# Kernel tuning notes

Measured on AMD Instinct MI355X. Metric: run time of the kernel, lower is better.

## Reference

```python
import jax, jax.numpy as jnp
import numpy as np

N_EL, N_NUC, N_UP = 768, 32, 384
EMB, EDGE_IN, TPS = 128, 32, 64
N_SAME = 2 * N_UP * (N_UP - 1)   # 294144
N_ANTI = 2 * N_UP * N_UP         # 294912
N_NE = N_NUC * N_EL              # 24576


def silu(x):
    return x * jax.nn.sigmoid(x)


def setup_inputs() -> dict:
    key = jax.random.key(0)
    ks = iter(jax.random.split(key, 32))
    r = lambda shape: jax.random.normal(next(ks), shape, jnp.float32)
    ri = lambda shape, hi: jax.random.randint(next(ks), shape, 0, hi, jnp.int32)
    return dict(
        electrons=r((N_EL, EMB)),
        nuclei=r((N_NUC, TPS)),
        feat_same=r((N_SAME, EDGE_IN)),
        feat_anti=r((N_ANTI, EDGE_IN)),
        feat_ne=r((N_NE, EDGE_IN)),
        senders_same=ri((N_SAME,), N_EL),
        receivers_same=ri((N_SAME,), N_EL),
        senders_anti=ri((N_ANTI,), N_EL),
        receivers_anti=ri((N_ANTI,), N_EL),
        senders_ne=ri((N_NE,), N_NUC),
        receivers_ne=ri((N_NE,), N_EL),
        # stacked subnet params, edge-type order: (same, anti, ne)
        u_W=r((3, EDGE_IN, TPS)) * 0.1, u_b=r((3, TPS)) * 0.1,
        w_W=r((3, TPS, TPS)) * 0.1, w_b=r((3, TPS)) * 0.1,
        h_W_ee=r((2, EMB, TPS)) * 0.1, h_b_ee=r((2, TPS)) * 0.1,  # same, anti
        h_W_ne=r((TPS, TPS)) * 0.1, h_b_ne=r((TPS,)) * 0.1,
        g_W_res=r((EMB, EMB)) * 0.1, g_b_res=r((EMB,)) * 0.1,
        g_W_z=r((3, TPS, EMB)) * 0.1, g_b_z=r((3, EMB)) * 0.1,
    )


def reference(electrons, nuclei, feat_same, feat_anti, feat_ne,
              senders_same, receivers_same, senders_anti, receivers_anti,
              senders_ne, receivers_ne,
              u_W, u_b, w_W, w_b, h_W_ee, h_b_ee, h_W_ne, h_b_ne,
              g_W_res, g_b_res, g_W_z, g_b_z):
    n_el = electrons.shape[0]
    feats = (feat_same, feat_anti, feat_ne)
    senders = (senders_same, senders_anti, senders_ne)
    receivers = (receivers_same, receivers_anti, receivers_ne)
    # h subnet applied to sender node data (electrons for same/anti, nuclei for ne)
    hx_nodes = (
        silu(electrons @ h_W_ee[0] + h_b_ee[0]),
        silu(electrons @ h_W_ee[1] + h_b_ee[1]),
        silu(nuclei @ h_W_ne + h_b_ne),
    )
    z = []
    for t in range(3):  # fixed structural loop over edge types
        e = silu(feats[t] @ u_W[t] + u_b[t])     # deep edge features: u[typ]
        we = silu(e @ w_W[t] + w_b[t])           # w[typ](edge.features)
        msg = we * hx_nodes[t][senders[t]]       # convolution: gather + elementwise
        z.append(jax.ops.segment_sum(msg, receivers[t], num_segments=n_el))
    # featurewise update rule: g_residual(electrons) + sum_typ g_typ(z[typ])
    updated = silu(electrons @ g_W_res + g_b_res)
    for t in range(3):
        updated = updated + silu(z[t] @ g_W_z[t] + g_b_z[t])
    # residual connection on electron embeddings
    return updated + electrons
```

## Files before the change

### kernel.cpp

```cpp
#include <hip/hip_runtime.h>
#include <hip/hip_bf16.h>
#include <stdint.h>

#define N_ELx 768
#define EMBx 128
#define TPSx 64
#define EDGE_INx 32
#define EPB 512
#define NBINS 2304
#define NB_SORT 96

typedef __attribute__((ext_vector_type(8))) short bf16x8;
typedef __attribute__((ext_vector_type(4))) float f32x4;
typedef __attribute__((ext_vector_type(4))) uint32_t u32x4;

__device__ __forceinline__ short f2bf(float f) {
    union { float f; uint32_t u; } v; v.f = f;
    uint32_t u = v.u;
    uint32_t r = (u + 0x7FFFu + ((u >> 16) & 1u)) >> 16;
    return (short)r;
}

__device__ __forceinline__ uint32_t cvtpk(float lo, float hi) {
    uint32_t r;
    asm("v_cvt_pk_bf16_f32 %0, %1, %2" : "=v"(r) : "v"(lo), "v"(hi));
    return r;
}

__device__ __forceinline__ bf16x8 mk8(uint32_t a, uint32_t b, uint32_t c, uint32_t d) {
    union { u32x4 u; bf16x8 h; } x;
    x.u = (u32x4){a, b, c, d};
    return x.h;
}

__device__ __forceinline__ float silu_f(float x) {
    float e = __builtin_amdgcn_exp2f(-1.442695041f * x);
    return x * __builtin_amdgcn_rcpf(1.0f + e);
}

__global__ __launch_bounds__(256)
void setup_kernel(const float* __restrict__ elec, const float* __restrict__ nuclei,
                  const float* __restrict__ uW, const float* __restrict__ wW,
                  const float* __restrict__ hWee, const float* __restrict__ hbee,
                  const float* __restrict__ hWne, const float* __restrict__ hbne,
                  float* __restrict__ hx0, float* __restrict__ hx1, float* __restrict__ hxn,
                  short* __restrict__ ufragT, short* __restrict__ wWfrag,
                  const int* __restrict__ r0, const int* __restrict__ r1,
                  const int* __restrict__ r2,
                  int n0, int n1, int n2, int* __restrict__ blockHist,
                  float* __restrict__ z)
{
    __shared__ __align__(16) char smem[32768];
    int b = blockIdx.x;
    int tid = threadIdx.x;
    if (b < 12) {
        short* lds_a = (short*)smem;
        int t = b / 6, rb = b % 6;
        const float* W = hWee + t * (128 * 64);
        {
            int row = tid >> 1, half = tid & 1;
            const float4* src = (const float4*)(elec + (size_t)(rb * 128 + row) * 128 + half * 64);
            #pragma unroll
            for (int c = 0; c < 8; ++c) {
                float4 fa = src[c * 2 + 0], fb = src[c * 2 + 1];
                bf16x8 v;
                v[0] = f2bf(fa.x); v[1] = f2bf(fa.y); v[2] = f2bf(fa.z); v[3] = f2bf(fa.w);
                v[4] = f2bf(fb.x); v[5] = f2bf(fb.y); v[6] = f2bf(fb.z); v[7] = f2bf(fb.w);
                int kk = half * 2 + (c >> 2), kc = c & 3;
                *(bf16x8*)&lds_a[((kk * 4 + kc) * 128 + row) * 8] = v;
            }
        }
        __syncthreads();
        int lane = tid & 63, w = tid >> 6, kc = lane >> 4, cr = lane & 15;
        int col = w * 16 + cr;
        bf16x8 bfrag[4];
        #pragma unroll
        for (int kk = 0; kk < 4; ++kk) {
            bf16x8 v;
            #pragma unroll
            for (int j = 0; j < 8; ++j)
                v[j] = f2bf(W[(kk * 32 + kc * 8 + j) * 64 + col]);
            bfrag[kk] = v;
        }
        float bias = hbee[t * 64 + col];
        float* dst = (t == 0 ? hx0 : hx1);
        f32x4 zero4 = {0.f, 0.f, 0.f, 0.f};
        #pragma unroll
        for (int rt = 0; rt < 8; ++rt) {
            f32x4 acc = zero4;
            #pragma unroll
            for (int kk = 0; kk < 4; ++kk) {
                bf16x8 a = *(const bf16x8*)&lds_a[((kk * 4 + kc) * 128 + rt * 16 + cr) * 8];
                acc = __builtin_amdgcn_mfma_f32_16x16x32_bf16(a, bfrag[kk], acc, 0, 0, 0);
            }
            #pragma unroll
            for (int r = 0; r < 4; ++r) {
                int row = rb * 128 + rt * 16 + kc * 4 + r;
                dst[row * 64 + col] = silu_f(acc[r] + bias);
            }
        }
    } else if (b == 12) {
        int lr = tid >> 6, col = tid & 63;
        for (int i = 0; i < 8; ++i) {
            int row = lr * 8 + i;
            float acc = 0.f;
            for (int k = 0; k < 64; ++k)
                acc += nuclei[row * 64 + k] * hWne[k * 64 + col];
            hxn[row * 64 + col] = silu_f(acc + hbne[col]);
        }
    } else if (b == 13) {
        for (int idx = tid; idx < 3 * 4 * 64; idx += 256) {
            int lane = idx & 63, tr = (idx >> 6) & 3, ty = idx >> 8;
            int lg = lane >> 4, cr = lane & 15;
            for (int j = 0; j < 8; ++j)
                ufragT[idx * 8 + j] =
                    f2bf(uW[(ty * EDGE_INx + lg * 8 + j) * TPSx + tr * 16 + cr]);
        }
        for (int idx = tid; idx < 3 * 2 * 4 * 64; idx += 256) {
            int lane = idx & 63, ct = (idx >> 6) & 3, ks = (idx >> 8) & 1, ty = idx >> 9;
            for (int j = 0; j < 8; ++j) {
                int k = ks * 32 + (lane >> 4) * 8 + j, col = ct * 16 + (lane & 15);
                wWfrag[idx * 8 + j] = f2bf(wW[(ty * 64 + k) * 64 + col]);
            }
        }
    } else {
        int* h = (int*)smem;
        int bb = b - 14;
        for (int i = bb * 256 + tid; i < 3 * N_ELx * TPSx; i += NB_SORT * 256)
            z[i] = 0.f;
        for (int i = tid; i < NBINS; i += 256) h[i] = 0;
        __syncthreads();
        int total = n0 + n1 + n2;
        int chunk = (total + NB_SORT - 1) / NB_SORT;
        int start = bb * chunk, end = min(start + chunk, total);
        for (int i = start + tid; i < end; i += 256) {
            int t, j;
            if (i < n0)            { t = 0; j = i; }
            else if (i < n0 + n1)  { t = 1; j = i - n0; }
            else                   { t = 2; j = i - n0 - n1; }
            int rv = (t == 0 ? r0 : (t == 1 ? r1 : r2))[j];
            atomicAdd(&h[t * 768 + rv], 1);
        }
        __syncthreads();
        for (int i = tid; i < NBINS; i += 256)
            blockHist[i * NB_SORT + bb] = h[i];
    }
}

__global__ __launch_bounds__(256)
void binscan_kernel(int* __restrict__ blockHist, int* __restrict__ binTotal)
{
    int bin = blockIdx.x * 256 + threadIdx.x;
    int* p = blockHist + bin * NB_SORT;
    int run = 0;
    for (int b = 0; b < NB_SORT; ++b) { int v = p[b]; p[b] = run; run += v; }
    binTotal[bin] = run;
}

__global__ __launch_bounds__(256)
void scatter2_kernel(const int* __restrict__ r0, const int* __restrict__ r1,
                     const int* __restrict__ r2,
                     int n0, int n1, int n2,
                     const int* __restrict__ blockHist,
                     const int* __restrict__ binTotal,
                     int* __restrict__ perm)
{
    __shared__ int cursor[NBINS];
    __shared__ int part[256];
    int tid = threadIdx.x, b = blockIdx.x;
    int l[9]; int s = 0;
    #pragma unroll
    for (int j = 0; j < 9; ++j) { l[j] = binTotal[tid * 9 + j]; s += l[j]; }
    part[tid] = s;
    __syncthreads();
    for (int off = 1; off < 256; off <<= 1) {
        int v = (tid >= off) ? part[tid - off] : 0;
        __syncthreads();
        part[tid] += v;
        __syncthreads();
    }
    int run = (tid == 0) ? 0 : part[tid - 1];
    #pragma unroll
    for (int j = 0; j < 9; ++j) {
        int bin = tid * 9 + j;
        cursor[bin] = run + blockHist[bin * NB_SORT + b];
        run += l[j];
    }
    __syncthreads();
    int total = n0 + n1 + n2;
    int chunk = (total + NB_SORT - 1) / NB_SORT;
    int start = b * chunk, end = min(start + chunk, total);
    for (int i = start + tid; i < end; i += 256) {
        int t, j;
        if (i < n0)            { t = 0; j = i; }
        else if (i < n0 + n1)  { t = 1; j = i - n0; }
        else                   { t = 2; j = i - n0 - n1; }
        int rv = (t == 0 ? r0 : (t == 1 ? r1 : r2))[j];
        int pos = atomicAdd(&cursor[t * 768 + rv], 1);
        perm[pos] = j;
    }
}

__global__ __launch_bounds__(256)
void edge_kernel(const float* __restrict__ feat0, const float* __restrict__ feat1,
                 const float* __restrict__ feat2,
                 const int* __restrict__ s0, const int* __restrict__ s1, const int* __restrict__ s2,
                 const int* __restrict__ r0, const int* __restrict__ r1, const int* __restrict__ r2,
                 const float* __restrict__ u_b, const float* __restrict__ w_b,
                 const float* __restrict__ hx0, const float* __restrict__ hx1,
                 const float* __restrict__ hxn,
                 const short* __restrict__ ufragT, const short* __restrict__ wWfrag,
                 const int* __restrict__ perm,
                 float* __restrict__ z,
                 int n0, int n1, int n2, int nb0, int nb1)
{
    int b = blockIdx.x;
    int t; const float* feat; const int* sn; const int* rc; const float* hx; int nE;
    if (b < nb0)            { t = 0; feat = feat0; sn = s0; rc = r0; hx = hx0; nE = n0; }
    else if (b < nb0 + nb1) { t = 1; b -= nb0; feat = feat1; sn = s1; rc = r1; hx = hx1; nE = n1; }
    else                    { t = 2; b -= nb0 + nb1; feat = feat2; sn = s2; rc = r2; hx = hxn; nE = n2; }

    int tid = threadIdx.x;
    int w = tid >> 6, lane = tid & 63, lg = lane >> 4, cr = lane & 15;
    int ebase = b * EPB + w * 128;
    if (ebase >= nE) return;
    bool partial = (ebase + 128 > nE);
    int t_off = (t == 0) ? 0 : (t == 1 ? n0 : n0 + n1);
    float* zt = z + t * (N_ELx * TPSx);

    bf16x8 uf[4];
    #pragma unroll
    for (int tr = 0; tr < 4; ++tr)
        uf[tr] = *(const bf16x8*)(ufragT + ((t * 4 + tr) * 64 + lane) * 8);
    bf16x8 wf[4][2];
    #pragma unroll
    for (int tn = 0; tn < 4; ++tn)
        #pragma unroll
        for (int ks = 0; ks < 2; ++ks)
            wf[tn][ks] = *(const bf16x8*)(wWfrag + (((t * 2 + ks) * 4 + tn) * 64 + lane) * 8);
    float4 ubv[4];
    #pragma unroll
    for (int tr = 0; tr < 4; ++tr)
        ubv[tr] = *(const float4*)(u_b + t * 64 + tr * 16 + lg * 4);
    float wbv[4];
    #pragma unroll
    for (int tn = 0; tn < 4; ++tn)
        wbv[tn] = w_b[t * 64 + tn * 16 + cr];

    int pe_own0, pe_own1, s_own0, s_own1, r_own0, r_own1;
    {
        int e0i = ebase + lane;
        int e1i = ebase + 64 + lane;
        pe_own0 = perm[t_off + min(e0i, nE - 1)];
        pe_own1 = perm[t_off + min(e1i, nE - 1)];
        s_own0 = sn[pe_own0]; r_own0 = rc[pe_own0];
        s_own1 = sn[pe_own1]; r_own1 = rc[pe_own1];
    }

    const int srcA = ((lg & 1) * 2) * 16 + cr;
    const int srcB = srcA + 16;
    const bool selLow = (lg < 2);
    f32x4 zero4 = {0.f, 0.f, 0.f, 0.f};

    float accv[4] = {0.f, 0.f, 0.f, 0.f};
    int curR = -1;
    auto flush = [&]() {
        if (curR >= 0) {
            #pragma unroll
            for (int tn = 0; tn < 4; ++tn) {
                float v = accv[tn];
                v += __shfl_xor(v, 16, 64);
                v += __shfl_xor(v, 32, 64);
                if (lg == 0) atomicAdd(&zt[curR * 64 + tn * 16 + cr], v);
                accv[tn] = 0.f;
            }
        }
    };

    int pF_n = __shfl(pe_own0, cr, 64);
    float4 fa_n, fc_n;
    {
        const float4* fp = (const float4*)(feat + (size_t)pF_n * EDGE_INx + lg * 8);
        fa_n = fp[0]; fc_n = fp[1];
    }

    #pragma unroll 2
    for (int tc = 0; tc < 8; ++tc) {
        int slot_hi = (tc & 4);
        int b16 = (tc & 3) * 16;
        float4 fa = fa_n, fc = fc_n;

        if (tc < 7) {
            int ntc = tc + 1;
            int npe = ((ntc & 4)) ? pe_own1 : pe_own0;
            pF_n = __shfl(npe, ((ntc & 3) * 16) + cr, 64);
            const float4* fp = (const float4*)(feat + (size_t)pF_n * EDGE_INx + lg * 8);
            fa_n = fp[0]; fc_n = fp[1];
        }

        int s_cur = slot_hi ? s_own1 : s_own0;
        int r_cur = slot_hi ? r_own1 : r_own0;
        int sidv[4];
        #pragma unroll
        for (int r = 0; r < 4; ++r)
            sidv[r] = __shfl(s_cur, b16 + lg * 4 + r, 64);
        int rF = __shfl(r_cur, b16, 64);
        int rL = __shfl(r_cur, b16 + 15, 64);

        float hv[4][4];
        if (!partial) {
            #pragma unroll
            for (int r = 0; r < 4; ++r) {
                const float* hp = hx + sidv[r] * TPSx + cr;
                #pragma unroll
                for (int tn = 0; tn < 4; ++tn)
                    hv[tn][r] = hp[tn * 16];
            }
        } else {
            #pragma unroll
            for (int r = 0; r < 4; ++r) {
                bool aE = (ebase + tc * 16 + lg * 4 + r) < nE;
                const float* hp = hx + sidv[r] * TPSx + cr;
                #pragma unroll
                for (int tn = 0; tn < 4; ++tn)
                    hv[tn][r] = aE ? hp[tn * 16] : 0.f;
            }
        }

        bf16x8 fB = mk8(cvtpk(fa.x, fa.y), cvtpk(fa.z, fa.w),
                        cvtpk(fc.x, fc.y), cvtpk(fc.z, fc.w));

        f32x4 d1[4];
        #pragma unroll
        for (int tr = 0; tr < 4; ++tr)
            d1[tr] = __builtin_amdgcn_mfma_f32_16x16x32_bf16(uf[tr], fB, zero4, 0, 0, 0);

        uint32_t pk1[4][2];
        #pragma unroll
        for (int tr = 0; tr < 4; ++tr) {
            float v0 = silu_f(d1[tr][0] + ubv[tr].x);
            float v1 = silu_f(d1[tr][1] + ubv[tr].y);
            float v2 = silu_f(d1[tr][2] + ubv[tr].z);
            float v3 = silu_f(d1[tr][3] + ubv[tr].w);
            pk1[tr][0] = cvtpk(v0, v1);
            pk1[tr][1] = cvtpk(v2, v3);
        }

        bf16x8 ebf[2];
        #pragma unroll
        for (int ks = 0; ks < 2; ++ks) {
            int t0 = 2 * ks, t1 = 2 * ks + 1;
            uint32_t a0 = (uint32_t)__shfl((int)pk1[t0][0], srcA, 64);
            uint32_t b0 = (uint32_t)__shfl((int)pk1[t1][0], srcA, 64);
            uint32_t a1 = (uint32_t)__shfl((int)pk1[t0][1], srcA, 64);
            uint32_t b1 = (uint32_t)__shfl((int)pk1[t1][1], srcA, 64);
            uint32_t a2 = (uint32_t)__shfl((int)pk1[t0][0], srcB, 64);
            uint32_t b2 = (uint32_t)__shfl((int)pk1[t1][0], srcB, 64);
            uint32_t a3 = (uint32_t)__shfl((int)pk1[t0][1], srcB, 64);
            uint32_t b3 = (uint32_t)__shfl((int)pk1[t1][1], srcB, 64);
            ebf[ks] = mk8(selLow ? a0 : b0, selLow ? a1 : b1,
                          selLow ? a2 : b2, selLow ? a3 : b3);
        }

        f32x4 d2[4];
        #pragma unroll
        for (int tn = 0; tn < 4; ++tn) {
            f32x4 acc = __builtin_amdgcn_mfma_f32_16x16x32_bf16(ebf[0], wf[tn][0], zero4, 0, 0, 0);
            d2[tn] = __builtin_amdgcn_mfma_f32_16x16x32_bf16(ebf[1], wf[tn][1], acc, 0, 0, 0);
        }

        float m[4][4];
        #pragma unroll
        for (int tn = 0; tn < 4; ++tn)
            #pragma unroll
            for (int r = 0; r < 4; ++r)
                m[tn][r] = silu_f(d2[tn][r] + wbv[tn]) * hv[tn][r];

        if (rF == rL) {
            if (rF != curR) { flush(); curR = rF; }
            #pragma unroll
            for (int tn = 0; tn < 4; ++tn)
                accv[tn] += (m[tn][0] + m[tn][1]) + (m[tn][2] + m[tn][3]);
        } else {
            flush();
            curR = -1;
            int ridv[4];
            #pragma unroll
            for (int r = 0; r < 4; ++r)
                ridv[r] = __shfl(r_cur, b16 + lg * 4 + r, 64);
            float a0 = m[0][0], a1 = m[1][0], a2 = m[2][0], a3 = m[3][0];
            int segR = ridv[0];
            #pragma unroll
            for (int r = 1; r < 4; ++r) {
                if (ridv[r] != segR) {
                    atomicAdd(&zt[segR * 64 +  0 + cr], a0);
                    atomicAdd(&zt[segR * 64 + 16 + cr], a1);
                    atomicAdd(&zt[segR * 64 + 32 + cr], a2);
                    atomicAdd(&zt[segR * 64 + 48 + cr], a3);
                    a0 = m[0][r]; a1 = m[1][r]; a2 = m[2][r]; a3 = m[3][r];
                    segR = ridv[r];
                } else {
                    a0 += m[0][r]; a1 += m[1][r]; a2 += m[2][r]; a3 += m[3][r];
                }
            }
            atomicAdd(&zt[segR * 64 +  0 + cr], a0);
            atomicAdd(&zt[segR * 64 + 16 + cr], a1);
            atomicAdd(&zt[segR * 64 + 32 + cr], a2);
            atomicAdd(&zt[segR * 64 + 48 + cr], a3);
        }
    }
    flush();
}

__global__ __launch_bounds__(128)
void final_kernel(const float* __restrict__ elec, const float* __restrict__ z,
                  const float* __restrict__ gWres, const float* __restrict__ gbres,
                  const float* __restrict__ gWz, const float* __restrict__ gbz,
                  float* __restrict__ out)
{
    __shared__ float xe[4 * 128];
    __shared__ float xz[3 * 4 * 64];
    int b = blockIdx.x;
    int tid = threadIdx.x;
    int row0 = b * 4;
    for (int i = tid; i < 4 * 128; i += 128)
        xe[i] = elec[row0 * 128 + i];
    for (int i = tid; i < 3 * 4 * 64; i += 128) {
        int t = i >> 8; int rr = (i >> 6) & 3; int k = i & 63;
        xz[i] = z[t * N_ELx * 64 + (row0 + rr) * 64 + k];
    }
    __syncthreads();

    int col = tid;
    float accr[4] = {0.f, 0.f, 0.f, 0.f};
    for (int k = 0; k < 128; ++k) {
        float wv = gWres[k * 128 + col];
        #pragma unroll
        for (int r = 0; r < 4; ++r) accr[r] += xe[r * 128 + k] * wv;
    }
    float o[4];
    float br = gbres[col];
    #pragma unroll
    for (int r = 0; r < 4; ++r) o[r] = silu_f(accr[r] + br) + xe[r * 128 + col];

    for (int t = 0; t < 3; ++t) {
        float accz[4] = {0.f, 0.f, 0.f, 0.f};
        for (int k = 0; k < 64; ++k) {
            float wv = gWz[(t * 64 + k) * 128 + col];
            #pragma unroll
            for (int r = 0; r < 4; ++r) accz[r] += xz[t * 256 + r * 64 + k] * wv;
        }
        float bz = gbz[t * 128 + col];
        #pragma unroll
        for (int r = 0; r < 4; ++r) o[r] += silu_f(accz[r] + bz);
    }
    #pragma unroll
    for (int r = 0; r < 4; ++r) out[(row0 + r) * 128 + col] = o[r];
}

extern "C" void kernel_launch(void* const* d_in, const int* in_sizes, int n_in,
                              void* d_out, int out_size, void* d_ws, size_t ws_size,
                              hipStream_t stream)
{
    const float* elec   = (const float*)d_in[0];
    const float* nuclei = (const float*)d_in[1];
    const float* feat0  = (const float*)d_in[2];
    const float* feat1  = (const float*)d_in[3];
    const float* feat2  = (const float*)d_in[4];
    const int*   s0     = (const int*)d_in[5];
    const int*   r0     = (const int*)d_in[6];
    const int*   s1     = (const int*)d_in[7];
    const int*   r1     = (const int*)d_in[8];
    const int*   s2     = (const int*)d_in[9];
    const int*   r2     = (const int*)d_in[10];
    const float* u_W    = (const float*)d_in[11];
    const float* u_b    = (const float*)d_in[12];
    const float* w_W    = (const float*)d_in[13];
    const float* w_b    = (const float*)d_in[14];
    const float* hWee   = (const float*)d_in[15];
    const float* hbee   = (const float*)d_in[16];
    const float* hWne   = (const float*)d_in[17];
    const float* hbne   = (const float*)d_in[18];
    const float* gWres  = (const float*)d_in[19];
    const float* gbres  = (const float*)d_in[20];
    const float* gWz    = (const float*)d_in[21];
    const float* gbz    = (const float*)d_in[22];
    float* out = (float*)d_out;

    char* ws = (char*)d_ws;
    float* hx0      = (float*)(ws + 0);
    float* hx1      = (float*)(ws + 196608);
    float* hxn      = (float*)(ws + 393216);
    float* z        = (float*)(ws + 401408);
    short* ufragT   = (short*)(ws + 991232);
    short* wWfrag   = (short*)(ws + 1003520);
    int*   binTotal = (int*)(ws + 1028096);
    int*   perm     = (int*)(ws + 1046528);
    int*   blockHist= (int*)(ws + 3501056);

    int n0 = in_sizes[2] / EDGE_INx;
    int n1 = in_sizes[3] / EDGE_INx;
    int n2 = in_sizes[4] / EDGE_INx;
    int nb0 = (n0 + EPB - 1) / EPB;
    int nb1 = (n1 + EPB - 1) / EPB;
    int nb2 = (n2 + EPB - 1) / EPB;

    setup_kernel<<<14 + NB_SORT, 256, 0, stream>>>(
        elec, nuclei, u_W, w_W, hWee, hbee, hWne, hbne,
        hx0, hx1, hxn, ufragT, wWfrag,
        r0, r1, r2, n0, n1, n2, blockHist, z);
    binscan_kernel<<<NBINS / 256, 256, 0, stream>>>(blockHist, binTotal);
    scatter2_kernel<<<NB_SORT, 256, 0, stream>>>(r0, r1, r2, n0, n1, n2,
                                                 blockHist, binTotal, perm);
    edge_kernel<<<nb0 + nb1 + nb2, 256, 0, stream>>>(
        feat0, feat1, feat2, s0, s1, s2, r0, r1, r2,
        u_b, w_b, hx0, hx1, hxn, ufragT, wWfrag, perm, z,
        n0, n1, n2, nb0, nb1);
    final_kernel<<<192, 128, 0, stream>>>(elec, z, gWres, gbres, gWz, gbz, out);
}
```

Measured before the change: 102.5 us.

## Parallelize bin scan per wave, halve edges per wave, use LDS transpose

The bin prefix scan now gives each bin a whole wave and uses shuffle-based scans, where before one thread walked 96 entries serially. The edge kernel processes 64 edges per wave instead of 128, doubling the number of blocks. It also replaces the 16-shuffle register transpose of the first-layer activations with a write and read through a small per-wave LDS buffer. More blocks repeat the per-block weight-fragment loads, and the LDS round trip adds latency within each wave.

```diff
diff --git a/kernel.cpp b/kernel.cpp
--- a/kernel.cpp
+++ b/kernel.cpp
@@ -6,13 +6,14 @@
 #define EMBx 128
 #define TPSx 64
 #define EDGE_INx 32
-#define EPB 512
+#define EPB 256
 #define NBINS 2304
 #define NB_SORT 96
 
 typedef __attribute__((ext_vector_type(8))) short bf16x8;
 typedef __attribute__((ext_vector_type(4))) float f32x4;
 typedef __attribute__((ext_vector_type(4))) uint32_t u32x4;
+typedef __attribute__((ext_vector_type(2))) uint32_t u32x2;
 
 __device__ __forceinline__ short f2bf(float f) {
     union { float f; uint32_t u; } v; v.f = f;
@@ -150,11 +151,27 @@
 __global__ __launch_bounds__(256)
 void binscan_kernel(int* __restrict__ blockHist, int* __restrict__ binTotal)
 {
-    int bin = blockIdx.x * 256 + threadIdx.x;
+    int tid = threadIdx.x;
+    int w = tid >> 6, lane = tid & 63;
+    int bin = blockIdx.x * 4 + w;
     int* p = blockHist + bin * NB_SORT;
-    int run = 0;
-    for (int b = 0; b < NB_SORT; ++b) { int v = p[b]; p[b] = run; run += v; }
-    binTotal[bin] = run;
+    int a = p[lane];
+    int bv = (lane < 32) ? p[64 + lane] : 0;
+    int a0 = a, b0 = bv;
+    #pragma unroll
+    for (int d = 1; d < 64; d <<= 1) {
+        int tv = __shfl_up(a, d, 64);
+        if (lane >= d) a += tv;
+    }
+    int sumA = __shfl(a, 63, 64);
+    #pragma unroll
+    for (int d = 1; d < 32; d <<= 1) {
+        int tv = __shfl_up(bv, d, 64);
+        if (lane >= d) bv += tv;
+    }
+    p[lane] = a - a0;
+    if (lane < 32) p[64 + lane] = sumA + bv - b0;
+    if (lane == 31) binTotal[bin] = sumA + bv;
 }
 
 __global__ __launch_bounds__(256)
@@ -214,6 +231,8 @@
                  float* __restrict__ z,
                  int n0, int n1, int n2, int nb0, int nb1)
 {
+    __shared__ __align__(16) char ebuf_all[4][16 * 144];
+
     int b = blockIdx.x;
     int t; const float* feat; const int* sn; const int* rc; const float* hx; int nE;
     if (b < nb0)            { t = 0; feat = feat0; sn = s0; rc = r0; hx = hx0; nE = n0; }
@@ -222,9 +241,10 @@
 
     int tid = threadIdx.x;
     int w = tid >> 6, lane = tid & 63, lg = lane >> 4, cr = lane & 15;
-    int ebase = b * EPB + w * 128;
+    int ebase = b * EPB + w * 64;
     if (ebase >= nE) return;
-    bool partial = (ebase + 128 > nE);
+    bool partial = (ebase + 64 > nE);
+    char* ebuf = ebuf_all[w];
     int t_off = (t == 0) ? 0 : (t == 1 ? n0 : n0 + n1);
     float* zt = z + t * (N_ELx * TPSx);
 
@@ -247,19 +267,11 @@
     for (int tn = 0; tn < 4; ++tn)
         wbv[tn] = w_b[t * 64 + tn * 16 + cr];
 
-    int pe_own0, pe_own1, s_own0, s_own1, r_own0, r_own1;
-    {
-        int e0i = ebase + lane;
-        int e1i = ebase + 64 + lane;
-        pe_own0 = perm[t_off + min(e0i, nE - 1)];
-        pe_own1 = perm[t_off + min(e1i, nE - 1)];
-        s_own0 = sn[pe_own0]; r_own0 = rc[pe_own0];
-        s_own1 = sn[pe_own1]; r_own1 = rc[pe_own1];
-    }
-
-    const int srcA = ((lg & 1) * 2) * 16 + cr;
-    const int srcB = srcA + 16;
-    const bool selLow = (lg < 2);
+    int e_own = ebase + lane;
+    int pe_own = perm[t_off + min(e_own, nE - 1)];
+    int s_own = sn[pe_own];
+    int r_own = rc[pe_own];
+
     f32x4 zero4 = {0.f, 0.f, 0.f, 0.f};
 
     float accv[4] = {0.f, 0.f, 0.f, 0.f};
@@ -277,7 +289,7 @@
         }
     };
 
-    int pF_n = __shfl(pe_own0, cr, 64);
+    int pF_n = __shfl(pe_own, cr, 64);
     float4 fa_n, fc_n;
     {
         const float4* fp = (const float4*)(feat + (size_t)pF_n * EDGE_INx + lg * 8);
@@ -285,27 +297,22 @@
     }
 
     #pragma unroll 2
-    for (int tc = 0; tc < 8; ++tc) {
-        int slot_hi = (tc & 4);
-        int b16 = (tc & 3) * 16;
+    for (int tc = 0; tc < 4; ++tc) {
+        int b16 = tc * 16;
         float4 fa = fa_n, fc = fc_n;
 
-        if (tc < 7) {
-            int ntc = tc + 1;
-            int npe = ((ntc & 4)) ? pe_own1 : pe_own0;
-            pF_n = __shfl(npe, ((ntc & 3) * 16) + cr, 64);
+        if (tc < 3) {
+            pF_n = __shfl(pe_own, (tc + 1) * 16 + cr, 64);
             const float4* fp = (const float4*)(feat + (size_t)pF_n * EDGE_INx + lg * 8);
             fa_n = fp[0]; fc_n = fp[1];
         }
 
-        int s_cur = slot_hi ? s_own1 : s_own0;
-        int r_cur = slot_hi ? r_own1 : r_own0;
         int sidv[4];
         #pragma unroll
         for (int r = 0; r < 4; ++r)
-            sidv[r] = __shfl(s_cur, b16 + lg * 4 + r, 64);
-        int rF = __shfl(r_cur, b16, 64);
-        int rL = __shfl(r_cur, b16 + 15, 64);
+            sidv[r] = __shfl(s_own, b16 + lg * 4 + r, 64);
+        int rF = __shfl(r_own, b16, 64);
+        int rL = __shfl(r_own, b16 + 15, 64);
 
         float hv[4][4];
         if (!partial) {
@@ -319,7 +326,7 @@
         } else {
             #pragma unroll
             for (int r = 0; r < 4; ++r) {
-                bool aE = (ebase + tc * 16 + lg * 4 + r) < nE;
+                bool aE = (ebase + b16 + lg * 4 + r) < nE;
                 const float* hp = hx + sidv[r] * TPSx + cr;
                 #pragma unroll
                 for (int tn = 0; tn < 4; ++tn)
@@ -335,38 +342,24 @@
         for (int tr = 0; tr < 4; ++tr)
             d1[tr] = __builtin_amdgcn_mfma_f32_16x16x32_bf16(uf[tr], fB, zero4, 0, 0, 0);
 
-        uint32_t pk1[4][2];
         #pragma unroll
         for (int tr = 0; tr < 4; ++tr) {
             float v0 = silu_f(d1[tr][0] + ubv[tr].x);
             float v1 = silu_f(d1[tr][1] + ubv[tr].y);
             float v2 = silu_f(d1[tr][2] + ubv[tr].z);
             float v3 = silu_f(d1[tr][3] + ubv[tr].w);
-            pk1[tr][0] = cvtpk(v0, v1);
-            pk1[tr][1] = cvtpk(v2, v3);
-        }
-
-        bf16x8 ebf[2];
-        #pragma unroll
-        for (int ks = 0; ks < 2; ++ks) {
-            int t0 = 2 * ks, t1 = 2 * ks + 1;
-            uint32_t a0 = (uint32_t)__shfl((int)pk1[t0][0], srcA, 64);
-            uint32_t b0 = (uint32_t)__shfl((int)pk1[t1][0], srcA, 64);
-            uint32_t a1 = (uint32_t)__shfl((int)pk1[t0][1], srcA, 64);
-            uint32_t b1 = (uint32_t)__shfl((int)pk1[t1][1], srcA, 64);
-            uint32_t a2 = (uint32_t)__shfl((int)pk1[t0][0], srcB, 64);
-            uint32_t b2 = (uint32_t)__shfl((int)pk1[t1][0], srcB, 64);
-            uint32_t a3 = (uint32_t)__shfl((int)pk1[t0][1], srcB, 64);
-            uint32_t b3 = (uint32_t)__shfl((int)pk1[t1][1], srcB, 64);
-            ebf[ks] = mk8(selLow ? a0 : b0, selLow ? a1 : b1,
-                          selLow ? a2 : b2, selLow ? a3 : b3);
-        }
+            u32x2 pk; pk[0] = cvtpk(v0, v1); pk[1] = cvtpk(v2, v3);
+            *(u32x2*)(ebuf + cr * 144 + tr * 32 + lg * 8) = pk;
+        }
+
+        bf16x8 ebf0 = *(const bf16x8*)(ebuf + cr * 144 + 0 * 64 + lg * 16);
+        bf16x8 ebf1 = *(const bf16x8*)(ebuf + cr * 144 + 1 * 64 + lg * 16);
 
         f32x4 d2[4];
         #pragma unroll
         for (int tn = 0; tn < 4; ++tn) {
-            f32x4 acc = __builtin_amdgcn_mfma_f32_16x16x32_bf16(ebf[0], wf[tn][0], zero4, 0, 0, 0);
-            d2[tn] = __builtin_amdgcn_mfma_f32_16x16x32_bf16(ebf[1], wf[tn][1], acc, 0, 0, 0);
+            f32x4 acc = __builtin_amdgcn_mfma_f32_16x16x32_bf16(ebf0, wf[tn][0], zero4, 0, 0, 0);
+            d2[tn] = __builtin_amdgcn_mfma_f32_16x16x32_bf16(ebf1, wf[tn][1], acc, 0, 0, 0);
         }
 
         float m[4][4];
@@ -387,7 +380,7 @@
             int ridv[4];
             #pragma unroll
             for (int r = 0; r < 4; ++r)
-                ridv[r] = __shfl(r_cur, b16 + lg * 4 + r, 64);
+                ridv[r] = __shfl(r_own, b16 + lg * 4 + r, 64);
             float a0 = m[0][0], a1 = m[1][0], a2 = m[2][0], a3 = m[3][0];
             int segR = ridv[0];
             #pragma unroll
@@ -509,7 +502,7 @@
         elec, nuclei, u_W, w_W, hWee, hbee, hWne, hbne,
         hx0, hx1, hxn, ufragT, wWfrag,
         r0, r1, r2, n0, n1, n2, blockHist, z);
-    binscan_kernel<<<NBINS / 256, 256, 0, stream>>>(blockHist, binTotal);
+    binscan_kernel<<<NBINS / 4, 256, 0, stream>>>(blockHist, binTotal);
     scatter2_kernel<<<NB_SORT, 256, 0, stream>>>(r0, r1, r2, n0, n1, n2,
                                                  blockHist, binTotal, perm);
     edge_kernel<<<nb0 + nb1 + nb2, 256, 0, stream>>>(
```

Result: faster. 90.89 us (-11.3%).
